# Performance work log

Measured on AMD Instinct MI355X. Metric: run time of the kernel, lower is better.

Reference implementation:

```python
import jax, jax.numpy as jnp
import numpy as np

B = 1024          # batch
H = 512           # hidden_dim
T = 256           # seq_len
CD = 2            # coord_dim
LAT = 64 + 64 + 128  # total latent dim


def setup_inputs() -> dict:
    key = jax.random.key(0)
    ks = jax.random.split(key, 20)
    s = 0.05  # weight init scale
    rn = lambda k, shp: (jax.random.normal(k, shp, dtype=jnp.float32) * s)
    return {
        "z_primitive": jax.random.normal(ks[0], (B, 64), dtype=jnp.float32),
        "z_skill": jax.random.normal(ks[1], (B, 64), dtype=jnp.float32),
        "z_style": jax.random.normal(ks[2], (B, 128), dtype=jnp.float32),
        "W_proj": rn(ks[3], (2 * H, LAT)),
        "b_proj": jnp.zeros((2 * H,), jnp.float32),
        "Wih1": rn(ks[4], (4 * H, CD)),
        "Whh1": rn(ks[5], (4 * H, H)),
        "bih1": jnp.zeros((4 * H,), jnp.float32),
        "bhh1": jnp.zeros((4 * H,), jnp.float32),
        "Wih2": rn(ks[6], (4 * H, H)),
        "Whh2": rn(ks[7], (4 * H, H)),
        "bih2": jnp.zeros((4 * H,), jnp.float32),
        "bhh2": jnp.zeros((4 * H,), jnp.float32),
        "Wo1": rn(ks[8], (H // 2, H)),
        "bo1": jnp.zeros((H // 2,), jnp.float32),
        "Wo2": rn(ks[9], (CD, H // 2)),
        "bo2": jnp.zeros((CD,), jnp.float32),
    }


def _lstm_cell(x, h, c, Wih, Whh, bih, bhh):
    # PyTorch gate order: i, f, g, o
    gates = x @ Wih.T + h @ Whh.T + (bih + bhh)
    i, f, g, o = jnp.split(gates, 4, axis=1)
    c_new = jax.nn.sigmoid(f) * c + jax.nn.sigmoid(i) * jnp.tanh(g)
    h_new = jax.nn.sigmoid(o) * jnp.tanh(c_new)
    return h_new, c_new


def reference(z_primitive, z_skill, z_style, W_proj, b_proj,
              Wih1, Whh1, bih1, bhh1, Wih2, Whh2, bih2, bhh2,
              Wo1, bo1, Wo2, bo2):
    z = jnp.concatenate([z_primitive, z_skill, z_style], axis=1)  # [B, LAT]
    init = z @ W_proj.T + b_proj                                  # [B, 2H]
    h0 = init[:, :H]
    c0 = init[:, H:]
    x0 = jnp.zeros((z.shape[0], CD), init.dtype)

    def step(carry, _):
        x, h1, c1, h2, c2 = carry
        h1, c1 = _lstm_cell(x, h1, c1, Wih1, Whh1, bih1, bhh1)
        h2, c2 = _lstm_cell(h1, h2, c2, Wih2, Whh2, bih2, bhh2)
        # output MLP (Dropout inactive in eval)
        y = jax.nn.relu(h2 @ Wo1.T + bo1) @ Wo2.T + bo2  # [B, CD]
        return (y, h1, c1, h2, c2), y

    # h0/c0 repeated across both LSTM layers (repeat(2,1,1) in torch)
    _, ys = jax.lax.scan(step, (x0, h0, c0, h0, c0), None, length=T)
    return jnp.transpose(ys, (1, 0, 2))  # [B, T, CD]
```

## Files before the change

### kernel.cpp

```cpp
#include <hip/hip_runtime.h>
#include <math.h>

#define NB 1024
#define NH 512
#define NT 256
#define NCD 2

typedef unsigned short u16;
typedef __bf16 bf16x8 __attribute__((ext_vector_type(8)));
typedef float  f32x4  __attribute__((ext_vector_type(4)));

#define MFMA_BF16 __builtin_amdgcn_mfma_f32_16x16x32_bf16

__device__ __forceinline__ float sigf(float x) { return 1.0f / (1.0f + expf(-x)); }
__device__ __forceinline__ float b2f(u16 u) {
    union { unsigned i; float f; } v; v.i = ((unsigned)u) << 16; return v.f;
}
__device__ __forceinline__ u16 f2b(float f) {
    union { float f; unsigned i; } v; v.f = f;
    unsigned r = v.i + 0x7fffu + ((v.i >> 16) & 1u);
    return (u16)(r >> 16);
}

__device__ __forceinline__ void async_cp16(const void* gptr, void* lptr) {
    __builtin_amdgcn_global_load_lds(
        (const __attribute__((address_space(1))) unsigned int*)gptr,
        (__attribute__((address_space(3))) unsigned int*)lptr,
        16, 0, 0);
}

__global__ __launch_bounds__(256) void convert3(
    const float* __restrict__ a, const float* __restrict__ b,
    const float* __restrict__ c,
    u16* __restrict__ oa, u16* __restrict__ ob, u16* __restrict__ oc)
{
    const int i = blockIdx.x * 256 + threadIdx.x;
    oa[i] = f2b(a[i]); ob[i] = f2b(b[i]); oc[i] = f2b(c[i]);
}

__global__ __launch_bounds__(256) void convw1(
    const float* __restrict__ a, u16* __restrict__ o)
{
    const int i = blockIdx.x * 256 + threadIdx.x;
    o[i] = f2b(a[i]);
}

__global__ __launch_bounds__(256) void bsum_k(
    const float* __restrict__ bi1, const float* __restrict__ bh1,
    const float* __restrict__ bi2, const float* __restrict__ bh2,
    float* __restrict__ o1, float* __restrict__ o2)
{
    const int i = blockIdx.x * 256 + threadIdx.x;
    o1[i] = bi1[i] + bh1[i];
    o2[i] = bi2[i] + bh2[i];
}

__global__ __launch_bounds__(256) void init_kernel(
    const float* __restrict__ zp, const float* __restrict__ zs,
    const float* __restrict__ zst, const float* __restrict__ Wp,
    const float* __restrict__ bp,
    u16* __restrict__ h1, float* __restrict__ c1,
    u16* __restrict__ h2, float* __restrict__ c2)
{
    __shared__ float z[4][256];
    const int tid = threadIdx.x;
    const int b0  = blockIdx.x * 4;
    for (int i = tid; i < 4 * 256; i += 256) {
        const int bb = i >> 8, k = i & 255;
        float v;
        if (k < 64)       v = zp [(b0 + bb) * 64  + k];
        else if (k < 128) v = zs [(b0 + bb) * 64  + (k - 64)];
        else              v = zst[(b0 + bb) * 128 + (k - 128)];
        z[bb][k] = v;
    }
    __syncthreads();
    for (int rt = 0; rt < 4; ++rt) {
        const int r = rt * 256 + tid;
        const float bias = bp[r];
        float a0 = bias, a1 = bias, a2 = bias, a3 = bias;
        for (int k = 0; k < 256; ++k) {
            const float w = Wp[r * 256 + k];
            a0 += z[0][k] * w; a1 += z[1][k] * w;
            a2 += z[2][k] * w; a3 += z[3][k] * w;
        }
        const float acc[4] = {a0, a1, a2, a3};
        for (int bb = 0; bb < 4; ++bb) {
            const int b = b0 + bb;
            if (r < NH) {
                h1[b * NH + r] = f2b(acc[bb]);
                h2[b * NH + r] = f2b(acc[bb]);
            } else {
                c1[b * NH + r - NH] = acc[bb];
                c2[b * NH + r - NH] = acc[bb];
            }
        }
    }
}

__global__ __launch_bounds__(512, 4) void fused_out_lstm1(
    const u16* __restrict__ h2prev,
    const u16* __restrict__ A0,
    const u16* __restrict__ W0,
    const float* __restrict__ bsum,
    const float* __restrict__ Wx,
    const u16* __restrict__ W1b,
    const float* __restrict__ bo1, const float* __restrict__ Wo2,
    const float* __restrict__ bo2, float* __restrict__ outp,
    float* __restrict__ c, u16* __restrict__ hnext,
    const int t, const int do_lstm)
{
    __shared__ __align__(16) char smem[61440];
    float* eg  = (float*)smem;
    float* red = (float*)(smem + 36864);

    const int tid  = threadIdx.x;
    const int lane = tid & 63;
    const int wv   = tid >> 6;
    const int g    = wv & 3;
    const int mh   = wv >> 2;
    const int l15  = lane & 15;
    const int q    = lane >> 4;
    const int bx   = blockIdx.x;
    const int ut   = (bx & 7) * 2 + ((bx >> 3) & 1);
    const int grp  = bx >> 4;
    const int b0   = grp * 32;
    const int u0   = ut * 32;

    int goffW0, goffW1, goffA = 0, goffO[4];
    {
        const int c0 = (wv * 2) * 64 + lane;
        const int w0r = c0 >> 3;
        goffW0 = ((w0r >> 5) * NH + u0 + (w0r & 31)) * NH + (((c0 & 7) ^ (w0r & 7)) * 8);
        const int c1i = (wv * 2 + 1) * 64 + lane;
        const int w1r = c1i >> 3;
        goffW1 = ((w1r >> 5) * NH + u0 + (w1r & 31)) * NH + (((c1i & 7) ^ (w1r & 7)) * 8);
        if (wv < 4) {
            const int ca = wv * 64 + lane;
            const int ar = ca >> 3;
            goffA = (b0 + ar) * NH + (((ca & 7) ^ (ar & 7)) * 8);
        }
#pragma unroll
        for (int i = 0; i < 4; ++i) {
            const int cidx = (wv * 4 + i) * 64 + lane;
            const int row  = cidx >> 3;
            const int kc   = (cidx & 7) ^ (row & 7);
            goffO[i] = row * NH + kc * 8;
        }
    }

    auto issue = [&](int m, int bi) {
        const int k0 = (m & 7) * 64;
        char* base = smem + bi * 20480;
        async_cp16((const void*)(W0 + goffW0 + k0),
                   (void*)(base + 4096 + (wv * 2) * 1024));
        async_cp16((const void*)(W0 + goffW1 + k0),
                   (void*)(base + 4096 + (wv * 2 + 1) * 1024));
        if (wv < 4)
            async_cp16((const void*)(A0 + goffA + k0),
                       (void*)(base + wv * 1024));
    };

    const int u_e  = tid & 31;
    const int bq_e = tid >> 5;
    const int ug_e = u0 + u_e;
    float bs[4], wx0[4], wx1[4], cpre[2];
#pragma unroll
    for (int g4 = 0; g4 < 4; ++g4) bs[g4] = bsum[g4 * NH + ug_e];
#pragma unroll
    for (int g4 = 0; g4 < 4; ++g4) {
        wx0[g4] = Wx[(g4 * NH + ug_e) * 2 + 0];
        wx1[g4] = Wx[(g4 * NH + ug_e) * 2 + 1];
    }
    cpre[0] = c[(size_t)(b0 + bq_e * 2 + 0) * NH + ug_e];
    cpre[1] = c[(size_t)(b0 + bq_e * 2 + 1) * NH + ug_e];

    if (do_lstm) issue(0, 2);

    float r_x[4] = {0.f, 0.f, 0.f, 0.f};

    if (h2prev) {
        f32x4 acc_o[2][2];
#pragma unroll
        for (int mi = 0; mi < 2; ++mi)
#pragma unroll
            for (int ni = 0; ni < 2; ++ni)
                acc_o[mi][ni] = (f32x4){0.f, 0.f, 0.f, 0.f};

        for (int kk = 0; kk < 8; ++kk) {
            __syncthreads();
            const int k0 = kk * 64;
#pragma unroll
            for (int i = 0; i < 4; ++i)
                async_cp16((const void*)(W1b + goffO[i] + k0),
                           (void*)(smem + ((wv * 4 + i) << 10)));
            if (wv < 4)
                async_cp16((const void*)(h2prev + goffA + k0),
                           (void*)(smem + 32768 + (wv << 10)));
            asm volatile("s_waitcnt vmcnt(0)" ::: "memory");
            __builtin_amdgcn_s_barrier();
#pragma unroll
            for (int kh = 0; kh < 2; ++kh) {
                bf16x8 bfr[2], av[2];
#pragma unroll
                for (int ni = 0; ni < 2; ++ni) {
                    const int wrow = wv * 32 + ni * 16 + l15;
                    const int j = (kh * 4 + q) ^ (wrow & 7);
                    bfr[ni] = *(const bf16x8*)(smem + wrow * 128 + j * 16);
                }
#pragma unroll
                for (int mi = 0; mi < 2; ++mi) {
                    const int row = mi * 16 + l15;
                    const int j = (kh * 4 + q) ^ (row & 7);
                    av[mi] = *(const bf16x8*)(smem + 32768 + row * 128 + j * 16);
                }
#pragma unroll
                for (int mi = 0; mi < 2; ++mi)
#pragma unroll
                    for (int ni = 0; ni < 2; ++ni)
                        acc_o[mi][ni] = MFMA_BF16(av[mi], bfr[ni], acc_o[mi][ni], 0, 0, 0);
            }
        }
        float bo1n[2], w20[2], w21[2];
#pragma unroll
        for (int ni = 0; ni < 2; ++ni) {
            const int n = wv * 32 + ni * 16 + l15;
            bo1n[ni] = bo1[n]; w20[ni] = Wo2[n]; w21[ni] = Wo2[256 + n];
        }
        float pa[2][4], pb[2][4];
#pragma unroll
        for (int mi = 0; mi < 2; ++mi)
#pragma unroll
            for (int r = 0; r < 4; ++r) {
                const float s0 = fmaxf(acc_o[mi][0][r] + bo1n[0], 0.f);
                const float s1 = fmaxf(acc_o[mi][1][r] + bo1n[1], 0.f);
                pa[mi][r] = s0 * w20[0] + s1 * w20[1];
                pb[mi][r] = s0 * w21[0] + s1 * w21[1];
            }
#pragma unroll
        for (int off = 1; off < 16; off <<= 1)
#pragma unroll
            for (int mi = 0; mi < 2; ++mi)
#pragma unroll
                for (int r = 0; r < 4; ++r) {
                    pa[mi][r] += __shfl_xor(pa[mi][r], off, 64);
                    pb[mi][r] += __shfl_xor(pb[mi][r], off, 64);
                }
        if (l15 == 0) {
#pragma unroll
            for (int mi = 0; mi < 2; ++mi)
#pragma unroll
                for (int r = 0; r < 4; ++r) {
                    const int m = mi * 16 + q * 4 + r;
                    red[m * 16 + wv * 2 + 0] = pa[mi][r];
                    red[m * 16 + wv * 2 + 1] = pb[mi][r];
                }
        }
        __syncthreads();
        if (ut == 0 && tid < 64) {
            const int bl = tid >> 1, cc = tid & 1;
            float y = bo2[cc];
#pragma unroll
            for (int w8 = 0; w8 < 8; ++w8) y += red[bl * 16 + w8 * 2 + cc];
            outp[(size_t)(b0 + bl) * (NT * NCD) + (t - 1) * NCD + cc] = y;
        }
        if (do_lstm) {
            const int bq = tid >> 5;
#pragma unroll
            for (int jj = 0; jj < 2; ++jj)
#pragma unroll
                for (int cc = 0; cc < 2; ++cc) {
                    float y = bo2[cc];
#pragma unroll
                    for (int w8 = 0; w8 < 8; ++w8)
                        y += red[(bq * 2 + jj) * 16 + w8 * 2 + cc];
                    r_x[jj * 2 + cc] = y;
                }
        }
        __syncthreads();
    }
    if (!do_lstm) return;

    f32x4 acc[2];
    acc[0] = (f32x4){0.f, 0.f, 0.f, 0.f};
    acc[1] = (f32x4){0.f, 0.f, 0.f, 0.f};
    const int M = 8;
    issue(1, 0);
    int ci = 2;
    for (int m = 0; m < M; ++m) {
        if (m + 1 < M) {
            if (wv < 4) asm volatile("s_waitcnt vmcnt(3)" ::: "memory");
            else        asm volatile("s_waitcnt vmcnt(2)" ::: "memory");
        } else {
            asm volatile("s_waitcnt vmcnt(0)" ::: "memory");
        }
        __builtin_amdgcn_s_barrier();
        if (m + 2 < M) {
            int bi = ci + 2; if (bi >= 3) bi -= 3;
            issue(m + 2, bi);
        }
        const char* bA = smem + ci * 20480;
        const char* bW = bA + 4096;
#pragma unroll
        for (int khi = 0; khi < 2; ++khi) {
            bf16x8 bfr[2];
#pragma unroll
            for (int ni = 0; ni < 2; ++ni) {
                const int wrow = g * 32 + ni * 16 + l15;
                const int j = (khi * 4 + q) ^ (wrow & 7);
                bfr[ni] = *(const bf16x8*)(bW + wrow * 128 + j * 16);
            }
            const int row = mh * 16 + l15;
            const int j = (khi * 4 + q) ^ (row & 7);
            const bf16x8 av = *(const bf16x8*)(bA + row * 128 + j * 16);
            acc[0] = MFMA_BF16(av, bfr[0], acc[0], 0, 0, 0);
            acc[1] = MFMA_BF16(av, bfr[1], acc[1], 0, 0, 0);
        }
        ++ci; if (ci == 3) ci = 0;
    }

    __syncthreads();
#pragma unroll
    for (int ni = 0; ni < 2; ++ni)
#pragma unroll
        for (int r = 0; r < 4; ++r)
            eg[(g * 32 + mh * 16 + q * 4 + r) * 33 + ni * 16 + l15] = acc[ni][r];
    __syncthreads();

#pragma unroll
    for (int jj = 0; jj < 2; ++jj) {
        const int bl = bq_e * 2 + jj;
        const int b  = b0 + bl;
        float gv[4];
#pragma unroll
        for (int g4 = 0; g4 < 4; ++g4) gv[g4] = eg[(g4 * 32 + bl) * 33 + u_e] + bs[g4];
        const float x0 = r_x[jj * 2 + 0];
        const float x1 = r_x[jj * 2 + 1];
#pragma unroll
        for (int g4 = 0; g4 < 4; ++g4) gv[g4] += x0 * wx0[g4] + x1 * wx1[g4];
        const float iv = sigf(gv[0]);
        const float fv = sigf(gv[1]);
        const float gg = tanhf(gv[2]);
        const float ov = sigf(gv[3]);
        const size_t idx = (size_t)b * NH + ug_e;
        const float cn = fv * cpre[jj] + iv * gg;
        c[idx] = cn;
        hnext[idx] = f2b(ov * tanhf(cn));
    }
}

__global__ __launch_bounds__(512, 4) void lstm_mfma32(
    const u16* __restrict__ A0, const u16* __restrict__ W0,
    const u16* __restrict__ A1, const u16* __restrict__ W1,
    const float* __restrict__ bsum,
    float* __restrict__ c, u16* __restrict__ hnext,
    const int npass)
{
    __shared__ __align__(16) char smem[61440];
    float* eg = (float*)smem;

    const int tid  = threadIdx.x;
    const int lane = tid & 63;
    const int wv   = tid >> 6;
    const int g    = wv & 3;
    const int mh   = wv >> 2;
    const int l15  = lane & 15;
    const int q    = lane >> 4;
    const int bx   = blockIdx.x;
    const int ut   = (bx & 7) * 2 + ((bx >> 3) & 1);
    const int grp  = bx >> 4;
    const int b0   = grp * 32;
    const int u0   = ut * 32;

    int goffW0, goffW1, goffA = 0;
    {
        const int c0 = (wv * 2) * 64 + lane;
        const int w0r = c0 >> 3;
        goffW0 = ((w0r >> 5) * NH + u0 + (w0r & 31)) * NH + (((c0 & 7) ^ (w0r & 7)) * 8);
        const int c1i = (wv * 2 + 1) * 64 + lane;
        const int w1r = c1i >> 3;
        goffW1 = ((w1r >> 5) * NH + u0 + (w1r & 31)) * NH + (((c1i & 7) ^ (w1r & 7)) * 8);
        if (wv < 4) {
            const int ca = wv * 64 + lane;
            const int ar = ca >> 3;
            goffA = (b0 + ar) * NH + (((ca & 7) ^ (ar & 7)) * 8);
        }
    }

    const int u_e  = tid & 31;
    const int bq_e = tid >> 5;
    const int ug_e = u0 + u_e;
    float bs[4], cpre[2];
#pragma unroll
    for (int g4 = 0; g4 < 4; ++g4) bs[g4] = bsum[g4 * NH + ug_e];
    cpre[0] = c[(size_t)(b0 + bq_e * 2 + 0) * NH + ug_e];
    cpre[1] = c[(size_t)(b0 + bq_e * 2 + 1) * NH + ug_e];

    f32x4 acc[2];
    acc[0] = (f32x4){0.f, 0.f, 0.f, 0.f};
    acc[1] = (f32x4){0.f, 0.f, 0.f, 0.f};

    const int M = npass * 8;

    auto issue = [&](int m, int bi) {
        const u16* __restrict__ Ap = (m < 8) ? A0 : A1;
        const u16* __restrict__ Wp = (m < 8) ? W0 : W1;
        const int k0 = (m & 7) * 64;
        char* base = smem + bi * 20480;
        async_cp16((const void*)(Wp + goffW0 + k0),
                   (void*)(base + 4096 + (wv * 2) * 1024));
        async_cp16((const void*)(Wp + goffW1 + k0),
                   (void*)(base + 4096 + (wv * 2 + 1) * 1024));
        if (wv < 4)
            async_cp16((const void*)(Ap + goffA + k0),
                       (void*)(base + wv * 1024));
    };

    issue(0, 0);
    if (M > 1) issue(1, 1);
    int ci = 0;
    for (int m = 0; m < M; ++m) {
        if (m + 1 < M) {
            if (wv < 4) asm volatile("s_waitcnt vmcnt(3)" ::: "memory");
            else        asm volatile("s_waitcnt vmcnt(2)" ::: "memory");
        } else {
            asm volatile("s_waitcnt vmcnt(0)" ::: "memory");
        }
        __builtin_amdgcn_s_barrier();
        if (m + 2 < M) {
            int bi = ci + 2; if (bi >= 3) bi -= 3;
            issue(m + 2, bi);
        }
        const char* bA = smem + ci * 20480;
        const char* bW = bA + 4096;
#pragma unroll
        for (int khi = 0; khi < 2; ++khi) {
            bf16x8 bfr[2];
#pragma unroll
            for (int ni = 0; ni < 2; ++ni) {
                const int wrow = g * 32 + ni * 16 + l15;
                const int j = (khi * 4 + q) ^ (wrow & 7);
                bfr[ni] = *(const bf16x8*)(bW + wrow * 128 + j * 16);
            }
            const int row = mh * 16 + l15;
            const int j = (khi * 4 + q) ^ (row & 7);
            const bf16x8 av = *(const bf16x8*)(bA + row * 128 + j * 16);
            acc[0] = MFMA_BF16(av, bfr[0], acc[0], 0, 0, 0);
            acc[1] = MFMA_BF16(av, bfr[1], acc[1], 0, 0, 0);
        }
        ++ci; if (ci == 3) ci = 0;
    }

    __syncthreads();
#pragma unroll
    for (int ni = 0; ni < 2; ++ni)
#pragma unroll
        for (int r = 0; r < 4; ++r)
            eg[(g * 32 + mh * 16 + q * 4 + r) * 33 + ni * 16 + l15] = acc[ni][r];
    __syncthreads();

#pragma unroll
    for (int jj = 0; jj < 2; ++jj) {
        const int bl = bq_e * 2 + jj;
        const int b  = b0 + bl;
        float gv[4];
#pragma unroll
        for (int g4 = 0; g4 < 4; ++g4) gv[g4] = eg[(g4 * 32 + bl) * 33 + u_e] + bs[g4];
        const float iv = sigf(gv[0]);
        const float fv = sigf(gv[1]);
        const float gg = tanhf(gv[2]);
        const float ov = sigf(gv[3]);
        const size_t idx = (size_t)b * NH + ug_e;
        const float cn = fv * cpre[jj] + iv * gg;
        c[idx] = cn;
        hnext[idx] = f2b(ov * tanhf(cn));
    }
}

extern "C" void kernel_launch(void* const* d_in, const int* in_sizes, int n_in,
                              void* d_out, int out_size, void* d_ws, size_t ws_size,
                              hipStream_t stream)
{
    const float* zp   = (const float*)d_in[0];
    const float* zsk  = (const float*)d_in[1];
    const float* zst  = (const float*)d_in[2];
    const float* Wp   = (const float*)d_in[3];
    const float* bp   = (const float*)d_in[4];
    const float* Wih1 = (const float*)d_in[5];
    const float* Whh1 = (const float*)d_in[6];
    const float* bih1 = (const float*)d_in[7];
    const float* bhh1 = (const float*)d_in[8];
    const float* Wih2 = (const float*)d_in[9];
    const float* Whh2 = (const float*)d_in[10];
    const float* bih2 = (const float*)d_in[11];
    const float* bhh2 = (const float*)d_in[12];
    const float* Wo1  = (const float*)d_in[13];
    const float* bo1  = (const float*)d_in[14];
    const float* Wo2  = (const float*)d_in[15];
    const float* bo2  = (const float*)d_in[16];

    const size_t BH = (size_t)NB * NH;
    u16*   h1a   = (u16*)d_ws;
    u16*   h1b   = h1a + BH;
    u16*   h2a   = h1b + BH;
    u16*   h2b   = h2a + BH;
    float* c1    = (float*)(h2b + BH);
    float* c2    = c1 + BH;
    float* bs1   = c2 + BH;
    float* bs2   = bs1 + 2048;
    u16*   Wo1b  = (u16*)(bs2 + 2048);
    u16*   Whh1b = Wo1b + 131072;
    u16*   Wih2b = Whh1b + 1048576;
    u16*   Whh2b = Wih2b + 1048576;

    convert3<<<(2048 * 512) / 256, 256, 0, stream>>>(Whh1, Wih2, Whh2, Whh1b, Wih2b, Whh2b);
    convw1<<<(256 * 512) / 256, 256, 0, stream>>>(Wo1, Wo1b);
    bsum_k<<<2048 / 256, 256, 0, stream>>>(bih1, bhh1, bih2, bhh2, bs1, bs2);
    init_kernel<<<NB / 4, 256, 0, stream>>>(zp, zsk, zst, Wp, bp, h1a, c1, h2a, c2);

    u16* h1c = h1a; u16* h1n = h1b;
    u16* h2c = h2a; u16* h2n = h2b;
    float* outp = (float*)d_out;
    for (int t = 0; t < NT; ++t) {
        fused_out_lstm1<<<512, 512, 0, stream>>>(
            (t == 0) ? (const u16*)0 : h2c, h1c, Whh1b, bs1, Wih1,
            Wo1b, bo1, Wo2, bo2, outp, c1, h1n, t, 1);
        lstm_mfma32<<<512, 512, 0, stream>>>(h1n, Wih2b, h2c, Whh2b,
                                             bs2, c2, h2n, 2);
        u16* tmp = h1c; h1c = h1n; h1n = tmp;
        tmp = h2c; h2c = h2n; h2n = tmp;
    }
    fused_out_lstm1<<<512, 512, 0, stream>>>(
        h2c, h1c, Whh1b, bs1, Wih1,
        Wo1b, bo1, Wo2, bo2, outp, c1, h1n, NT, 0);
}
```

Baseline: 7.488 ms.

## Replace per-step kernel launches with persistent kernel using per-batch-group spin barriers

Fuses the 513 per-timestep launches into one persistent kernel of 512 blocks. Each 16-block batch group synchronizes through an atomic counter barrier, and the cell state stays in registers across steps. Hidden-state tiles are now read with agent-scope atomic loads into registers and then written to LDS, because async global-to-LDS copies would not see peer writes coherently. The intent is to remove launch overhead and inter-kernel gaps, at the risk of deadlock if not all 512 blocks are co-resident, and the spin loop carries a guard that could silently break correctness.

```diff
diff --git a/kernel.cpp b/kernel.cpp
--- a/kernel.cpp
+++ b/kernel.cpp
@@ -9,13 +9,11 @@
 typedef unsigned short u16;
 typedef __bf16 bf16x8 __attribute__((ext_vector_type(8)));
 typedef float  f32x4  __attribute__((ext_vector_type(4)));
+typedef unsigned int  u32x4 __attribute__((ext_vector_type(4)));
 
 #define MFMA_BF16 __builtin_amdgcn_mfma_f32_16x16x32_bf16
 
 __device__ __forceinline__ float sigf(float x) { return 1.0f / (1.0f + expf(-x)); }
-__device__ __forceinline__ float b2f(u16 u) {
-    union { unsigned i; float f; } v; v.i = ((unsigned)u) << 16; return v.f;
-}
 __device__ __forceinline__ u16 f2b(float f) {
     union { float f; unsigned i; } v; v.f = f;
     unsigned r = v.i + 0x7fffu + ((v.i >> 16) & 1u);
@@ -29,6 +27,16 @@
         16, 0, 0);
 }
 
+__device__ __forceinline__ u32x4 aload16(const u16* p) {
+    unsigned* q = (unsigned*)(void*)p;
+    u32x4 v;
+    v.x = __hip_atomic_load(q + 0, __ATOMIC_RELAXED, __HIP_MEMORY_SCOPE_AGENT);
+    v.y = __hip_atomic_load(q + 1, __ATOMIC_RELAXED, __HIP_MEMORY_SCOPE_AGENT);
+    v.z = __hip_atomic_load(q + 2, __ATOMIC_RELAXED, __HIP_MEMORY_SCOPE_AGENT);
+    v.w = __hip_atomic_load(q + 3, __ATOMIC_RELAXED, __HIP_MEMORY_SCOPE_AGENT);
+    return v;
+}
+
 __global__ __launch_bounds__(256) void convert3(
     const float* __restrict__ a, const float* __restrict__ b,
     const float* __restrict__ c,
@@ -53,6 +61,11 @@
     const int i = blockIdx.x * 256 + threadIdx.x;
     o1[i] = bi1[i] + bh1[i];
     o2[i] = bi2[i] + bh2[i];
+}
+
+__global__ __launch_bounds__(512) void zero_bar(unsigned* __restrict__ b)
+{
+    b[threadIdx.x] = 0u;
 }
 
 __global__ __launch_bounds__(256) void init_kernel(
@@ -97,21 +110,20 @@
     }
 }
 
-__global__ __launch_bounds__(512, 4) void fused_out_lstm1(
-    const u16* __restrict__ h2prev,
-    const u16* __restrict__ A0,
-    const u16* __restrict__ W0,
-    const float* __restrict__ bsum,
-    const float* __restrict__ Wx,
-    const u16* __restrict__ W1b,
-    const float* __restrict__ bo1, const float* __restrict__ Wo2,
-    const float* __restrict__ bo2, float* __restrict__ outp,
-    float* __restrict__ c, u16* __restrict__ hnext,
-    const int t, const int do_lstm)
+__global__ __launch_bounds__(512, 4) void decoder_persistent(
+    const u16* __restrict__ Whh1b, const u16* __restrict__ Wih2b,
+    const u16* __restrict__ Whh2b, const u16* __restrict__ Wo1b,
+    const float* __restrict__ bs1, const float* __restrict__ bs2,
+    const float* __restrict__ Wih1, const float* __restrict__ bo1,
+    const float* __restrict__ Wo2, const float* __restrict__ bo2,
+    const float* __restrict__ c1i, const float* __restrict__ c2i,
+    float* __restrict__ outp,
+    u16* h1A, u16* h1B, u16* h2A, u16* h2B,
+    unsigned* bar)
 {
     __shared__ __align__(16) char smem[61440];
     float* eg  = (float*)smem;
-    float* red = (float*)(smem + 36864);
+    float* red = (float*)(smem + 40960);
 
     const int tid  = threadIdx.x;
     const int lane = tid & 63;
@@ -131,9 +143,9 @@
         const int c0 = (wv * 2) * 64 + lane;
         const int w0r = c0 >> 3;
         goffW0 = ((w0r >> 5) * NH + u0 + (w0r & 31)) * NH + (((c0 & 7) ^ (w0r & 7)) * 8);
-        const int c1i = (wv * 2 + 1) * 64 + lane;
-        const int w1r = c1i >> 3;
-        goffW1 = ((w1r >> 5) * NH + u0 + (w1r & 31)) * NH + (((c1i & 7) ^ (w1r & 7)) * 8);
+        const int c1x = (wv * 2 + 1) * 64 + lane;
+        const int w1r = c1x >> 3;
+        goffW1 = ((w1r >> 5) * NH + u0 + (w1r & 31)) * NH + (((c1x & 7) ^ (w1r & 7)) * 8);
         if (wv < 4) {
             const int ca = wv * 64 + lane;
             const int ar = ca >> 3;
@@ -148,157 +160,46 @@
         }
     }
 
-    auto issue = [&](int m, int bi) {
-        const int k0 = (m & 7) * 64;
-        char* base = smem + bi * 20480;
-        async_cp16((const void*)(W0 + goffW0 + k0),
-                   (void*)(base + 4096 + (wv * 2) * 1024));
-        async_cp16((const void*)(W0 + goffW1 + k0),
-                   (void*)(base + 4096 + (wv * 2 + 1) * 1024));
-        if (wv < 4)
-            async_cp16((const void*)(A0 + goffA + k0),
-                       (void*)(base + wv * 1024));
-    };
-
     const int u_e  = tid & 31;
     const int bq_e = tid >> 5;
     const int ug_e = u0 + u_e;
-    float bs[4], wx0[4], wx1[4], cpre[2];
-#pragma unroll
-    for (int g4 = 0; g4 < 4; ++g4) bs[g4] = bsum[g4 * NH + ug_e];
+    float bs1r[4], bs2r[4], wx0[4], wx1[4];
 #pragma unroll
     for (int g4 = 0; g4 < 4; ++g4) {
-        wx0[g4] = Wx[(g4 * NH + ug_e) * 2 + 0];
-        wx1[g4] = Wx[(g4 * NH + ug_e) * 2 + 1];
+        bs1r[g4] = bs1[g4 * NH + ug_e];
+        bs2r[g4] = bs2[g4 * NH + ug_e];
+        wx0[g4]  = Wih1[(g4 * NH + ug_e) * 2 + 0];
+        wx1[g4]  = Wih1[(g4 * NH + ug_e) * 2 + 1];
     }
-    cpre[0] = c[(size_t)(b0 + bq_e * 2 + 0) * NH + ug_e];
-    cpre[1] = c[(size_t)(b0 + bq_e * 2 + 1) * NH + ug_e];
-
-    if (do_lstm) issue(0, 2);
-
-    float r_x[4] = {0.f, 0.f, 0.f, 0.f};
-
-    if (h2prev) {
-        f32x4 acc_o[2][2];
-#pragma unroll
-        for (int mi = 0; mi < 2; ++mi)
-#pragma unroll
-            for (int ni = 0; ni < 2; ++ni)
-                acc_o[mi][ni] = (f32x4){0.f, 0.f, 0.f, 0.f};
-
-        for (int kk = 0; kk < 8; ++kk) {
-            __syncthreads();
-            const int k0 = kk * 64;
-#pragma unroll
-            for (int i = 0; i < 4; ++i)
-                async_cp16((const void*)(W1b + goffO[i] + k0),
-                           (void*)(smem + ((wv * 4 + i) << 10)));
-            if (wv < 4)
-                async_cp16((const void*)(h2prev + goffA + k0),
-                           (void*)(smem + 32768 + (wv << 10)));
-            asm volatile("s_waitcnt vmcnt(0)" ::: "memory");
-            __builtin_amdgcn_s_barrier();
-#pragma unroll
-            for (int kh = 0; kh < 2; ++kh) {
-                bf16x8 bfr[2], av[2];
-#pragma unroll
-                for (int ni = 0; ni < 2; ++ni) {
-                    const int wrow = wv * 32 + ni * 16 + l15;
-                    const int j = (kh * 4 + q) ^ (wrow & 7);
-                    bfr[ni] = *(const bf16x8*)(smem + wrow * 128 + j * 16);
-                }
-#pragma unroll
-                for (int mi = 0; mi < 2; ++mi) {
-                    const int row = mi * 16 + l15;
-                    const int j = (kh * 4 + q) ^ (row & 7);
-                    av[mi] = *(const bf16x8*)(smem + 32768 + row * 128 + j * 16);
-                }
-#pragma unroll
-                for (int mi = 0; mi < 2; ++mi)
-#pragma unroll
-                    for (int ni = 0; ni < 2; ++ni)
-                        acc_o[mi][ni] = MFMA_BF16(av[mi], bfr[ni], acc_o[mi][ni], 0, 0, 0);
-            }
-        }
-        float bo1n[2], w20[2], w21[2];
-#pragma unroll
-        for (int ni = 0; ni < 2; ++ni) {
-            const int n = wv * 32 + ni * 16 + l15;
-            bo1n[ni] = bo1[n]; w20[ni] = Wo2[n]; w21[ni] = Wo2[256 + n];
-        }
-        float pa[2][4], pb[2][4];
-#pragma unroll
-        for (int mi = 0; mi < 2; ++mi)
-#pragma unroll
-            for (int r = 0; r < 4; ++r) {
-                const float s0 = fmaxf(acc_o[mi][0][r] + bo1n[0], 0.f);
-                const float s1 = fmaxf(acc_o[mi][1][r] + bo1n[1], 0.f);
-                pa[mi][r] = s0 * w20[0] + s1 * w20[1];
-                pb[mi][r] = s0 * w21[0] + s1 * w21[1];
-            }
-#pragma unroll
-        for (int off = 1; off < 16; off <<= 1)
-#pragma unroll
-            for (int mi = 0; mi < 2; ++mi)
-#pragma unroll
-                for (int r = 0; r < 4; ++r) {
-                    pa[mi][r] += __shfl_xor(pa[mi][r], off, 64);
-                    pb[mi][r] += __shfl_xor(pb[mi][r], off, 64);
-                }
-        if (l15 == 0) {
-#pragma unroll
-            for (int mi = 0; mi < 2; ++mi)
-#pragma unroll
-                for (int r = 0; r < 4; ++r) {
-                    const int m = mi * 16 + q * 4 + r;
-                    red[m * 16 + wv * 2 + 0] = pa[mi][r];
-                    red[m * 16 + wv * 2 + 1] = pb[mi][r];
-                }
-        }
-        __syncthreads();
-        if (ut == 0 && tid < 64) {
-            const int bl = tid >> 1, cc = tid & 1;
-            float y = bo2[cc];
-#pragma unroll
-            for (int w8 = 0; w8 < 8; ++w8) y += red[bl * 16 + w8 * 2 + cc];
-            outp[(size_t)(b0 + bl) * (NT * NCD) + (t - 1) * NCD + cc] = y;
-        }
-        if (do_lstm) {
-            const int bq = tid >> 5;
-#pragma unroll
-            for (int jj = 0; jj < 2; ++jj)
-#pragma unroll
-                for (int cc = 0; cc < 2; ++cc) {
-                    float y = bo2[cc];
-#pragma unroll
-                    for (int w8 = 0; w8 < 8; ++w8)
-                        y += red[(bq * 2 + jj) * 16 + w8 * 2 + cc];
-                    r_x[jj * 2 + cc] = y;
-                }
-        }
-        __syncthreads();
+    float c1r[2], c2r[2];
+    c1r[0] = c1i[(size_t)(b0 + bq_e * 2 + 0) * NH + ug_e];
+    c1r[1] = c1i[(size_t)(b0 + bq_e * 2 + 1) * NH + ug_e];
+    c2r[0] = c2i[(size_t)(b0 + bq_e * 2 + 0) * NH + ug_e];
+    c2r[1] = c2i[(size_t)(b0 + bq_e * 2 + 1) * NH + ug_e];
+    float bo1n[2], w20[2], w21[2];
+#pragma unroll
+    for (int ni = 0; ni < 2; ++ni) {
+        const int n = wv * 32 + ni * 16 + l15;
+        bo1n[ni] = bo1[n]; w20[ni] = Wo2[n]; w21[ni] = Wo2[256 + n];
     }
-    if (!do_lstm) return;
-
-    f32x4 acc[2];
-    acc[0] = (f32x4){0.f, 0.f, 0.f, 0.f};
-    acc[1] = (f32x4){0.f, 0.f, 0.f, 0.f};
-    const int M = 8;
-    issue(1, 0);
-    int ci = 2;
-    for (int m = 0; m < M; ++m) {
-        if (m + 1 < M) {
-            if (wv < 4) asm volatile("s_waitcnt vmcnt(3)" ::: "memory");
-            else        asm volatile("s_waitcnt vmcnt(2)" ::: "memory");
-        } else {
-            asm volatile("s_waitcnt vmcnt(0)" ::: "memory");
-        }
-        __builtin_amdgcn_s_barrier();
-        if (m + 2 < M) {
-            int bi = ci + 2; if (bi >= 3) bi -= 3;
-            issue(m + 2, bi);
-        }
-        const char* bA = smem + ci * 20480;
+    const float bo2c0 = bo2[0], bo2c1 = bo2[1];
+
+    u16 *h1c = h1A, *h1n = h1B, *h2c = h2A, *h2n = h2B;
+    unsigned  bar_target = 0;
+    unsigned* mybar = bar + grp * 16;
+
+    u32x4 rO0, rO1, rB0, rB1;
+
+    auto issueWB = [&](const u16* Wp, int m, int bi) {
+        const int k0 = (m & 7) * 64;
+        char* base = smem + bi * 20480;
+        async_cp16((const void*)(Wp + goffW0 + k0), (void*)(base + 4096 + (wv * 2) * 1024));
+        async_cp16((const void*)(Wp + goffW1 + k0), (void*)(base + 4096 + (wv * 2 + 1) * 1024));
+    };
+    auto awrite = [&](char* base, u32x4 v) {
+        *(u32x4*)(base + wv * 1024 + lane * 16) = v;
+    };
+    auto mstep = [&](const char* bA, f32x4* acc) {
         const char* bW = bA + 4096;
 #pragma unroll
         for (int khi = 0; khi < 2; ++khi) {
@@ -315,164 +216,238 @@
             acc[0] = MFMA_BF16(av, bfr[0], acc[0], 0, 0, 0);
             acc[1] = MFMA_BF16(av, bfr[1], acc[1], 0, 0, 0);
         }
-        ++ci; if (ci == 3) ci = 0;
-    }
-
-    __syncthreads();
-#pragma unroll
-    for (int ni = 0; ni < 2; ++ni)
-#pragma unroll
-        for (int r = 0; r < 4; ++r)
-            eg[(g * 32 + mh * 16 + q * 4 + r) * 33 + ni * 16 + l15] = acc[ni][r];
-    __syncthreads();
-
-#pragma unroll
-    for (int jj = 0; jj < 2; ++jj) {
-        const int bl = bq_e * 2 + jj;
-        const int b  = b0 + bl;
-        float gv[4];
-#pragma unroll
-        for (int g4 = 0; g4 < 4; ++g4) gv[g4] = eg[(g4 * 32 + bl) * 33 + u_e] + bs[g4];
-        const float x0 = r_x[jj * 2 + 0];
-        const float x1 = r_x[jj * 2 + 1];
-#pragma unroll
-        for (int g4 = 0; g4 < 4; ++g4) gv[g4] += x0 * wx0[g4] + x1 * wx1[g4];
-        const float iv = sigf(gv[0]);
-        const float fv = sigf(gv[1]);
-        const float gg = tanhf(gv[2]);
-        const float ov = sigf(gv[3]);
-        const size_t idx = (size_t)b * NH + ug_e;
-        const float cn = fv * cpre[jj] + iv * gg;
-        c[idx] = cn;
-        hnext[idx] = f2b(ov * tanhf(cn));
-    }
-}
-
-__global__ __launch_bounds__(512, 4) void lstm_mfma32(
-    const u16* __restrict__ A0, const u16* __restrict__ W0,
-    const u16* __restrict__ A1, const u16* __restrict__ W1,
-    const float* __restrict__ bsum,
-    float* __restrict__ c, u16* __restrict__ hnext,
-    const int npass)
-{
-    __shared__ __align__(16) char smem[61440];
-    float* eg = (float*)smem;
-
-    const int tid  = threadIdx.x;
-    const int lane = tid & 63;
-    const int wv   = tid >> 6;
-    const int g    = wv & 3;
-    const int mh   = wv >> 2;
-    const int l15  = lane & 15;
-    const int q    = lane >> 4;
-    const int bx   = blockIdx.x;
-    const int ut   = (bx & 7) * 2 + ((bx >> 3) & 1);
-    const int grp  = bx >> 4;
-    const int b0   = grp * 32;
-    const int u0   = ut * 32;
-
-    int goffW0, goffW1, goffA = 0;
-    {
-        const int c0 = (wv * 2) * 64 + lane;
-        const int w0r = c0 >> 3;
-        goffW0 = ((w0r >> 5) * NH + u0 + (w0r & 31)) * NH + (((c0 & 7) ^ (w0r & 7)) * 8);
-        const int c1i = (wv * 2 + 1) * 64 + lane;
-        const int w1r = c1i >> 3;
-        goffW1 = ((w1r >> 5) * NH + u0 + (w1r & 31)) * NH + (((c1i & 7) ^ (w1r & 7)) * 8);
+    };
+    auto grpbar = [&]() {
+        bar_target += 16;
+        __syncthreads();
+        if (tid == 0) {
+            __hip_atomic_fetch_add(mybar, 1u, __ATOMIC_RELAXED, __HIP_MEMORY_SCOPE_AGENT);
+            int guard = 0;
+            while (__hip_atomic_load(mybar, __ATOMIC_RELAXED, __HIP_MEMORY_SCOPE_AGENT)
+                       < bar_target && ++guard < (1 << 16)) {
+                __builtin_amdgcn_s_sleep(1);
+            }
+        }
+        __syncthreads();
+    };
+    auto cellEp = [&](f32x4* acc, const float* bsr, float* cr, u16* hdst,
+                      const float* rx) {
+        __syncthreads();
+#pragma unroll
+        for (int ni = 0; ni < 2; ++ni)
+#pragma unroll
+            for (int r = 0; r < 4; ++r)
+                eg[(g * 32 + mh * 16 + q * 4 + r) * 33 + ni * 16 + l15] = acc[ni][r];
+        __syncthreads();
+#pragma unroll
+        for (int jj = 0; jj < 2; ++jj) {
+            const int bl = bq_e * 2 + jj;
+            const int b  = b0 + bl;
+            float gv[4];
+#pragma unroll
+            for (int g4 = 0; g4 < 4; ++g4) {
+                gv[g4] = eg[(g4 * 32 + bl) * 33 + u_e] + bsr[g4];
+                if (rx) gv[g4] += rx[jj * 2 + 0] * wx0[g4] + rx[jj * 2 + 1] * wx1[g4];
+            }
+            const float iv = sigf(gv[0]);
+            const float fv = sigf(gv[1]);
+            const float gg = tanhf(gv[2]);
+            const float ov = sigf(gv[3]);
+            const float cn = fv * cr[jj] + iv * gg;
+            cr[jj] = cn;
+            const unsigned hb = (unsigned)f2b(ov * tanhf(cn));
+            const unsigned pr = (unsigned)__shfl_xor((int)hb, 1, 64);
+            if (!(u_e & 1))
+                __hip_atomic_store((unsigned*)(void*)(hdst + (size_t)b * NH + ug_e),
+                                   hb | (pr << 16),
+                                   __ATOMIC_RELAXED, __HIP_MEMORY_SCOPE_AGENT);
+        }
+    };
+
+    for (int t = 0; t <= NT; ++t) {
+        const bool do_l = (t < NT);
         if (wv < 4) {
-            const int ca = wv * 64 + lane;
-            const int ar = ca >> 3;
-            goffA = (b0 + ar) * NH + (((ca & 7) ^ (ar & 7)) * 8);
-        }
-    }
-
-    const int u_e  = tid & 31;
-    const int bq_e = tid >> 5;
-    const int ug_e = u0 + u_e;
-    float bs[4], cpre[2];
-#pragma unroll
-    for (int g4 = 0; g4 < 4; ++g4) bs[g4] = bsum[g4 * NH + ug_e];
-    cpre[0] = c[(size_t)(b0 + bq_e * 2 + 0) * NH + ug_e];
-    cpre[1] = c[(size_t)(b0 + bq_e * 2 + 1) * NH + ug_e];
-
-    f32x4 acc[2];
-    acc[0] = (f32x4){0.f, 0.f, 0.f, 0.f};
-    acc[1] = (f32x4){0.f, 0.f, 0.f, 0.f};
-
-    const int M = npass * 8;
-
-    auto issue = [&](int m, int bi) {
-        const u16* __restrict__ Ap = (m < 8) ? A0 : A1;
-        const u16* __restrict__ Wp = (m < 8) ? W0 : W1;
-        const int k0 = (m & 7) * 64;
-        char* base = smem + bi * 20480;
-        async_cp16((const void*)(Wp + goffW0 + k0),
-                   (void*)(base + 4096 + (wv * 2) * 1024));
-        async_cp16((const void*)(Wp + goffW1 + k0),
-                   (void*)(base + 4096 + (wv * 2 + 1) * 1024));
-        if (wv < 4)
-            async_cp16((const void*)(Ap + goffA + k0),
-                       (void*)(base + wv * 1024));
-    };
-
-    issue(0, 0);
-    if (M > 1) issue(1, 1);
-    int ci = 0;
-    for (int m = 0; m < M; ++m) {
-        if (m + 1 < M) {
-            if (wv < 4) asm volatile("s_waitcnt vmcnt(3)" ::: "memory");
-            else        asm volatile("s_waitcnt vmcnt(2)" ::: "memory");
-        } else {
-            asm volatile("s_waitcnt vmcnt(0)" ::: "memory");
-        }
-        __builtin_amdgcn_s_barrier();
-        if (m + 2 < M) {
-            int bi = ci + 2; if (bi >= 3) bi -= 3;
-            issue(m + 2, bi);
-        }
-        const char* bA = smem + ci * 20480;
-        const char* bW = bA + 4096;
-#pragma unroll
-        for (int khi = 0; khi < 2; ++khi) {
-            bf16x8 bfr[2];
-#pragma unroll
-            for (int ni = 0; ni < 2; ++ni) {
-                const int wrow = g * 32 + ni * 16 + l15;
-                const int j = (khi * 4 + q) ^ (wrow & 7);
-                bfr[ni] = *(const bf16x8*)(bW + wrow * 128 + j * 16);
-            }
-            const int row = mh * 16 + l15;
-            const int j = (khi * 4 + q) ^ (row & 7);
-            const bf16x8 av = *(const bf16x8*)(bA + row * 128 + j * 16);
-            acc[0] = MFMA_BF16(av, bfr[0], acc[0], 0, 0, 0);
-            acc[1] = MFMA_BF16(av, bfr[1], acc[1], 0, 0, 0);
-        }
-        ++ci; if (ci == 3) ci = 0;
-    }
-
-    __syncthreads();
-#pragma unroll
-    for (int ni = 0; ni < 2; ++ni)
-#pragma unroll
-        for (int r = 0; r < 4; ++r)
-            eg[(g * 32 + mh * 16 + q * 4 + r) * 33 + ni * 16 + l15] = acc[ni][r];
-    __syncthreads();
-
-#pragma unroll
-    for (int jj = 0; jj < 2; ++jj) {
-        const int bl = bq_e * 2 + jj;
-        const int b  = b0 + bl;
-        float gv[4];
-#pragma unroll
-        for (int g4 = 0; g4 < 4; ++g4) gv[g4] = eg[(g4 * 32 + bl) * 33 + u_e] + bs[g4];
-        const float iv = sigf(gv[0]);
-        const float fv = sigf(gv[1]);
-        const float gg = tanhf(gv[2]);
-        const float ov = sigf(gv[3]);
-        const size_t idx = (size_t)b * NH + ug_e;
-        const float cn = fv * cpre[jj] + iv * gg;
-        c[idx] = cn;
-        hnext[idx] = f2b(ov * tanhf(cn));
+            if (t > 0) rO0 = aload16(h2c + goffA);
+            if (do_l)  rB0 = aload16(h1c + goffA);
+        }
+        if (do_l) issueWB(Whh1b, 0, 2);
+
+        float r_x[4] = {0.f, 0.f, 0.f, 0.f};
+
+        if (t > 0) {
+            f32x4 acc_o[2][2];
+#pragma unroll
+            for (int mi = 0; mi < 2; ++mi)
+#pragma unroll
+                for (int ni = 0; ni < 2; ++ni)
+                    acc_o[mi][ni] = (f32x4){0.f, 0.f, 0.f, 0.f};
+
+            for (int kk = 0; kk < 8; ++kk) {
+                __syncthreads();
+#pragma unroll
+                for (int i = 0; i < 4; ++i)
+                    async_cp16((const void*)(Wo1b + goffO[i] + kk * 64),
+                               (void*)(smem + ((wv * 4 + i) << 10)));
+                char* aBase = smem + 32768 + (kk & 1) * 4096;
+                if (wv < 4) awrite(aBase, (kk & 1) ? rO1 : rO0);
+                asm volatile("s_waitcnt vmcnt(0) lgkmcnt(0)" ::: "memory");
+                __builtin_amdgcn_s_barrier();
+                if (wv < 4 && kk + 1 < 8) {
+                    if ((kk + 1) & 1) rO1 = aload16(h2c + goffA + (kk + 1) * 64);
+                    else              rO0 = aload16(h2c + goffA + (kk + 1) * 64);
+                }
+#pragma unroll
+                for (int kh = 0; kh < 2; ++kh) {
+                    bf16x8 bfr[2], av[2];
+#pragma unroll
+                    for (int ni = 0; ni < 2; ++ni) {
+                        const int wrow = wv * 32 + ni * 16 + l15;
+                        const int j = (kh * 4 + q) ^ (wrow & 7);
+                        bfr[ni] = *(const bf16x8*)(smem + wrow * 128 + j * 16);
+                    }
+#pragma unroll
+                    for (int mi = 0; mi < 2; ++mi) {
+                        const int row = mi * 16 + l15;
+                        const int j = (kh * 4 + q) ^ (row & 7);
+                        av[mi] = *(const bf16x8*)(aBase + row * 128 + j * 16);
+                    }
+#pragma unroll
+                    for (int mi = 0; mi < 2; ++mi)
+#pragma unroll
+                        for (int ni = 0; ni < 2; ++ni)
+                            acc_o[mi][ni] = MFMA_BF16(av[mi], bfr[ni], acc_o[mi][ni], 0, 0, 0);
+                }
+            }
+            float pa[2][4], pb[2][4];
+#pragma unroll
+            for (int mi = 0; mi < 2; ++mi)
+#pragma unroll
+                for (int r = 0; r < 4; ++r) {
+                    const float s0 = fmaxf(acc_o[mi][0][r] + bo1n[0], 0.f);
+                    const float s1 = fmaxf(acc_o[mi][1][r] + bo1n[1], 0.f);
+                    pa[mi][r] = s0 * w20[0] + s1 * w20[1];
+                    pb[mi][r] = s0 * w21[0] + s1 * w21[1];
+                }
+#pragma unroll
+            for (int off = 1; off < 16; off <<= 1)
+#pragma unroll
+                for (int mi = 0; mi < 2; ++mi)
+#pragma unroll
+                    for (int r = 0; r < 4; ++r) {
+                        pa[mi][r] += __shfl_xor(pa[mi][r], off, 64);
+                        pb[mi][r] += __shfl_xor(pb[mi][r], off, 64);
+                    }
+            if (l15 == 0) {
+#pragma unroll
+                for (int mi = 0; mi < 2; ++mi)
+#pragma unroll
+                    for (int r = 0; r < 4; ++r) {
+                        const int m = mi * 16 + q * 4 + r;
+                        red[m * 16 + wv * 2 + 0] = pa[mi][r];
+                        red[m * 16 + wv * 2 + 1] = pb[mi][r];
+                    }
+            }
+            __syncthreads();
+            if (ut == 0 && tid < 64) {
+                const int bl = tid >> 1, cc = tid & 1;
+                float y = cc ? bo2c1 : bo2c0;
+#pragma unroll
+                for (int w8 = 0; w8 < 8; ++w8) y += red[bl * 16 + w8 * 2 + cc];
+                outp[(size_t)(b0 + bl) * (NT * NCD) + (t - 1) * NCD + cc] = y;
+            }
+            if (do_l) {
+#pragma unroll
+                for (int jj = 0; jj < 2; ++jj)
+#pragma unroll
+                    for (int cc = 0; cc < 2; ++cc) {
+                        float y = cc ? bo2c1 : bo2c0;
+#pragma unroll
+                        for (int w8 = 0; w8 < 8; ++w8)
+                            y += red[(bq_e * 2 + jj) * 16 + w8 * 2 + cc];
+                        r_x[jj * 2 + cc] = y;
+                    }
+            }
+            __syncthreads();
+        }
+        if (!do_l) break;
+
+        {
+            f32x4 acc[2];
+            acc[0] = (f32x4){0.f, 0.f, 0.f, 0.f};
+            acc[1] = (f32x4){0.f, 0.f, 0.f, 0.f};
+            if (wv < 4) rB1 = aload16(h1c + goffA + 64);
+            issueWB(Whh1b, 1, 0);
+            if (wv < 4) {
+                awrite(smem + 2 * 20480, rB0);
+                awrite(smem + 0 * 20480, rB1);
+                rB0 = aload16(h1c + goffA + 128);
+            }
+            int ci = 2;
+            for (int m = 0; m < 8; ++m) {
+                if (m + 1 < 8) {
+                    if (wv < 4) asm volatile("s_waitcnt vmcnt(6) lgkmcnt(0)" ::: "memory");
+                    else        asm volatile("s_waitcnt vmcnt(2)" ::: "memory");
+                } else {
+                    asm volatile("s_waitcnt vmcnt(0) lgkmcnt(0)" ::: "memory");
+                }
+                __builtin_amdgcn_s_barrier();
+                if (m + 2 < 8) {
+                    int bi = ci + 2; if (bi >= 3) bi -= 3;
+                    if (wv < 4) awrite(smem + bi * 20480, (m & 1) ? rB1 : rB0);
+                    issueWB(Whh1b, m + 2, bi);
+                    if (wv < 4 && m + 3 < 8) {
+                        if (m & 1) rB0 = aload16(h1c + goffA + (m + 3) * 64);
+                        else       rB1 = aload16(h1c + goffA + (m + 3) * 64);
+                    }
+                }
+                mstep(smem + ci * 20480, acc);
+                ++ci; if (ci == 3) ci = 0;
+            }
+            cellEp(acc, bs1r, c1r, h1n, r_x);
+        }
+        grpbar();
+
+        {
+            f32x4 acc[2];
+            acc[0] = (f32x4){0.f, 0.f, 0.f, 0.f};
+            acc[1] = (f32x4){0.f, 0.f, 0.f, 0.f};
+            if (wv < 4) rB0 = aload16(h1n + goffA);
+            issueWB(Wih2b, 0, 0);
+            if (wv < 4) rB1 = aload16(h1n + goffA + 64);
+            issueWB(Wih2b, 1, 1);
+            if (wv < 4) {
+                awrite(smem + 0 * 20480, rB0);
+                awrite(smem + 1 * 20480, rB1);
+                rB0 = aload16(h1n + goffA + 128);
+            }
+            int ci = 0;
+            for (int m = 0; m < 16; ++m) {
+                if (m + 1 < 16) {
+                    if (wv < 4) asm volatile("s_waitcnt vmcnt(6) lgkmcnt(0)" ::: "memory");
+                    else        asm volatile("s_waitcnt vmcnt(2)" ::: "memory");
+                } else {
+                    asm volatile("s_waitcnt vmcnt(0) lgkmcnt(0)" ::: "memory");
+                }
+                __builtin_amdgcn_s_barrier();
+                if (m + 2 < 16) {
+                    int bi = ci + 2; if (bi >= 3) bi -= 3;
+                    if (wv < 4) awrite(smem + bi * 20480, (m & 1) ? rB1 : rB0);
+                    issueWB((m + 2 < 8) ? Wih2b : Whh2b, m + 2, bi);
+                    if (wv < 4 && m + 3 < 16) {
+                        const u16* Ap = (m + 3 < 8) ? h1n : h2c;
+                        const int k0 = ((m + 3) & 7) * 64;
+                        if (m & 1) rB0 = aload16(Ap + goffA + k0);
+                        else       rB1 = aload16(Ap + goffA + k0);
+                    }
+                }
+                mstep(smem + ci * 20480, acc);
+                ++ci; if (ci == 3) ci = 0;
+            }
+            cellEp(acc, bs2r, c2r, h2n, (const float*)0);
+        }
+        grpbar();
+
+        { u16* tp = h1c; h1c = h1n; h1n = tp; tp = h2c; h2c = h2n; h2n = tp; }
     }
 }
 
@@ -511,25 +486,15 @@
     u16*   Whh1b = Wo1b + 131072;
     u16*   Wih2b = Whh1b + 1048576;
     u16*   Whh2b = Wih2b + 1048576;
+    unsigned* bar = (unsigned*)(Whh2b + 1048576);
 
     convert3<<<(2048 * 512) / 256, 256, 0, stream>>>(Whh1, Wih2, Whh2, Whh1b, Wih2b, Whh2b);
     convw1<<<(256 * 512) / 256, 256, 0, stream>>>(Wo1, Wo1b);
     bsum_k<<<2048 / 256, 256, 0, stream>>>(bih1, bhh1, bih2, bhh2, bs1, bs2);
     init_kernel<<<NB / 4, 256, 0, stream>>>(zp, zsk, zst, Wp, bp, h1a, c1, h2a, c2);
-
-    u16* h1c = h1a; u16* h1n = h1b;
-    u16* h2c = h2a; u16* h2n = h2b;
-    float* outp = (float*)d_out;
-    for (int t = 0; t < NT; ++t) {
-        fused_out_lstm1<<<512, 512, 0, stream>>>(
-            (t == 0) ? (const u16*)0 : h2c, h1c, Whh1b, bs1, Wih1,
-            Wo1b, bo1, Wo2, bo2, outp, c1, h1n, t, 1);
-        lstm_mfma32<<<512, 512, 0, stream>>>(h1n, Wih2b, h2c, Whh2b,
-                                             bs2, c2, h2n, 2);
-        u16* tmp = h1c; h1c = h1n; h1n = tmp;
-        tmp = h2c; h2c = h2n; h2n = tmp;
-    }
-    fused_out_lstm1<<<512, 512, 0, stream>>>(
-        h2c, h1c, Whh1b, bs1, Wih1,
-        Wo1b, bo1, Wo2, bo2, outp, c1, h1n, NT, 0);
-}
+    zero_bar<<<1, 512, 0, stream>>>(bar);
+
+    decoder_persistent<<<512, 512, 0, stream>>>(
+        Whh1b, Wih2b, Whh2b, Wo1b, bs1, bs2, Wih1, bo1, Wo2, bo2,
+        c1, c2, (float*)d_out, h1a, h1b, h2a, h2b, bar);
+}
```

Result: slower. 14.77 ms (+97.3%).
